# Performance work log

Hardware: AMD Instinct MI355X
Metric: run time of the kernel (lower is better)

The kernel has to match this reference:

```python
import jax, jax.numpy as jnp
import numpy as np

B, D, H1, H2, J, Q, O = 32768, 35, 256, 256, 12, 7, 5


def setup_inputs() -> dict:
    key = jax.random.key(0)
    ks = jax.random.split(key, 16)
    s = 0.05
    inp = {
        "x": jax.random.uniform(ks[0], (B, D), dtype=jnp.float32),
        "judge_ids": jax.random.randint(ks[1], (B,), 0, J, dtype=jnp.int32),
        # shared layers
        "W1_w": jax.random.normal(ks[2], (H1, D + 1), jnp.float32) * s,
        "W1_b": jnp.zeros((H1,), jnp.float32),
        "W2_w": jax.random.normal(ks[3], (H2, H1 + 1), jnp.float32) * s,
        "W2_b": jnp.zeros((H2,), jnp.float32),
        # judge-specific layers (stacked over J experts)
        "W1a_w": jax.random.normal(ks[4], (J, H1, D + 1), jnp.float32) * s,
        "W1a_b": jnp.zeros((J, H1), jnp.float32),
        "W2a_w": jax.random.normal(ks[5], (J, H2, H1 + 1), jnp.float32) * s,
        "W2a_b": jnp.zeros((J, H2), jnp.float32),
        # per-question output heads (shared + judge-specific)
        "V_w": jax.random.normal(ks[6], (Q, O, H2 + 1), jnp.float32) * s,
        "V_b": jnp.zeros((Q, O), jnp.float32),
        "Va_w": jax.random.normal(ks[7], (J, Q, O, H2 + 1), jnp.float32) * s,
        "Va_b": jnp.zeros((J, Q, O), jnp.float32),
    }
    return inp


def _append_ones(a):
    return jnp.concatenate([a, jnp.ones((a.shape[0], 1), a.dtype)], axis=1)


def reference(x, judge_ids, W1_w, W1_b, W2_w, W2_b, W1a_w, W1a_b, W2a_w, W2a_b, V_w, V_b, Va_w, Va_b):
    ids = judge_ids.astype(jnp.int32)
    xb = _append_ones(x)                                   # (B, D+1)
    # layer 1: shared + judge-routed
    a1 = jnp.einsum('bi,jhi->bjh', xb, W1a_w)              # (B, J, H1)
    j1 = jnp.take_along_axis(a1, ids[:, None, None], axis=1)[:, 0] + W1a_b[ids]
    z1 = jax.nn.relu(xb @ W1_w.T + W1_b + j1)              # (B, H1)
    z1b = _append_ones(z1)                                 # (B, H1+1)
    # layer 2
    a2 = jnp.einsum('bh,jgh->bjg', z1b, W2a_w)             # (B, J, H2)
    j2 = jnp.take_along_axis(a2, ids[:, None, None], axis=1)[:, 0] + W2a_b[ids]
    z2 = jax.nn.relu(z1b @ W2_w.T + W2_b + j2)             # (B, H2)
    z2b = _append_ones(z2)                                 # (B, H2+1)
    # per-question heads
    shared = jnp.einsum('bh,qoh->bqo', z2b, V_w) + V_b     # (B, Q, O)
    aV = jnp.einsum('bh,jqoh->bjqo', z2b, Va_w)            # (B, J, Q, O)
    jV = jnp.take_along_axis(aV, ids[:, None, None, None], axis=1)[:, 0] + Va_b[ids]
    return jax.nn.softmax(shared + jV, axis=-1)            # (B, Q, O)
```

## Files before the change

kernel.cpp:

```cpp
#include <hip/hip_runtime.h>
#include <stdint.h>

#define B_N   32768
#define D_IN  35
#define NJ    12
#define NQ    7
#define NO    5
#define QO    35
#define TILE  32
#define MAXSLOTS (B_N + NJ*TILE)
#define MAXT     (MAXSLOTS/TILE)

typedef __bf16  v8bf  __attribute__((ext_vector_type(8)));
typedef float   f32x4 __attribute__((ext_vector_type(4)));

__device__ __forceinline__ unsigned short f2bf(float f) {
    unsigned int u = __builtin_bit_cast(unsigned int, f);
    u += 0x7FFFu + ((u >> 16) & 1u);
    return (unsigned short)(u >> 16);
}
__device__ __forceinline__ unsigned int pack2(float a, float b) {
    return (unsigned int)f2bf(a) | ((unsigned int)f2bf(b) << 16);
}

__global__ void k_prep(const int* __restrict__ ids,
                       const float* __restrict__ W1_w, const float* __restrict__ W1_b,
                       const float* __restrict__ W2_w, const float* __restrict__ W2_b,
                       const float* __restrict__ W1a_w, const float* __restrict__ W1a_b,
                       const float* __restrict__ W2a_w, const float* __restrict__ W2a_b,
                       const float* __restrict__ V_w,  const float* __restrict__ V_b,
                       const float* __restrict__ Va_w, const float* __restrict__ Va_b,
                       unsigned short* __restrict__ w1c, unsigned short* __restrict__ w2c,
                       unsigned short* __restrict__ vc,
                       float* __restrict__ bias1, float* __restrict__ bias2,
                       float* __restrict__ biasv,
                       int* __restrict__ cursor, int* __restrict__ ntiles,
                       int* __restrict__ tileExpert, int* __restrict__ perm)
{
    const int tid = blockIdx.x * blockDim.x + threadIdx.x;
    const int nth = gridDim.x * blockDim.x;

    for (int q = tid; q < NJ * 256 * 64; q += nth) {
        int k4 = (q & 63) << 2, h = (q >> 6) & 255, jj = q >> 14;
        const float* a = &W2_w[h * 257 + k4];
        const float* b = &W2a_w[(jj * 256 + h) * 257 + k4];
        ushort4 o;
        o.x = f2bf(a[0] + b[0]); o.y = f2bf(a[1] + b[1]);
        o.z = f2bf(a[2] + b[2]); o.w = f2bf(a[3] + b[3]);
        *(ushort4*)&w2c[(size_t)q << 2] = o;
    }
    for (int q = tid; q < NJ * 256 * 16; q += nth) {
        int k4 = (q & 15) << 2, h = (q >> 4) & 255, jj = q >> 12;
        ushort4 o;
        float v[4];
#pragma unroll
        for (int e = 0; e < 4; ++e) {
            int k = k4 + e;
            v[e] = (k < D_IN) ? (W1_w[h * 36 + k] + W1a_w[(jj * 256 + h) * 36 + k]) : 0.f;
        }
        o.x = f2bf(v[0]); o.y = f2bf(v[1]); o.z = f2bf(v[2]); o.w = f2bf(v[3]);
        *(ushort4*)&w1c[(size_t)q << 2] = o;
    }
    for (int q = tid; q < NJ * 48 * 64; q += nth) {
        int k4 = (q & 63) << 2, qo = (q >> 6) % 48, jj = q / (48 * 64);
        ushort4 o;
        if (qo < QO) {
            const float* a = &V_w[qo * 257 + k4];
            const float* b = &Va_w[(jj * QO + qo) * 257 + k4];
            o.x = f2bf(a[0] + b[0]); o.y = f2bf(a[1] + b[1]);
            o.z = f2bf(a[2] + b[2]); o.w = f2bf(a[3] + b[3]);
        } else {
            o.x = o.y = o.z = o.w = 0;
        }
        *(ushort4*)&vc[(size_t)q << 2] = o;
    }
    for (int i = tid; i < NJ * 256; i += nth) {
        int h = i & 255, jj = i >> 8;
        bias1[i] = W1_w[h * 36 + 35] + W1a_w[(jj * 256 + h) * 36 + 35] + W1_b[h] + W1a_b[i];
        bias2[i] = W2_w[h * 257 + 256] + W2a_w[(jj * 256 + h) * 257 + 256] + W2_b[h] + W2a_b[i];
    }
    for (int i = tid; i < NJ * 48; i += nth) {
        int qo = i % 48, jj = i / 48;
        float v = 0.f;
        if (qo < QO) v = V_w[qo * 257 + 256] + Va_w[(jj * QO + qo) * 257 + 256]
                       + V_b[qo] + Va_b[jj * QO + qo];
        biasv[i] = v;
    }

    if (blockIdx.x == 0) {
        __shared__ int lh[NJ];
        __shared__ int s_cur[NJ], s_cnt[NJ], s_nt[NJ], tb[NJ + 1];
        const int lt = threadIdx.x;
        if (lt < NJ) lh[lt] = 0;
        __syncthreads();
        const int4* ids4 = (const int4*)ids;
        for (int i = lt; i < B_N / 4; i += 256) {
            int4 v = ids4[i];
            atomicAdd(&lh[v.x], 1); atomicAdd(&lh[v.y], 1);
            atomicAdd(&lh[v.z], 1); atomicAdd(&lh[v.w], 1);
        }
        __syncthreads();
        if (lt == 0) {
            int off = 0, t = 0;
            for (int j = 0; j < NJ; ++j) {
                int c = lh[j];
                int nt = (c + TILE - 1) / TILE;
                cursor[j] = off;
                s_cur[j] = off; s_cnt[j] = c; s_nt[j] = nt; tb[j] = t;
                t += nt;
                off += nt * TILE;
            }
            tb[NJ] = t;
            ntiles[0] = t;
        }
        __syncthreads();
        const int ntot = tb[NJ];
        for (int tt = lt; tt < ntot; tt += 256) {
            int j = 0;
            while (tb[j + 1] <= tt) ++j;
            tileExpert[tt] = j;
        }
        for (int p = lt; p < NJ * TILE; p += 256) {
            int j = p >> 5, o = p & 31;
            int c = s_cnt[j];
            int padN = s_nt[j] * TILE - c;
            if (o < padN) perm[s_cur[j] + c + o] = -1;
        }
    }
}

__global__ void k_scatter(const int* __restrict__ ids, int* __restrict__ cursor,
                          int* __restrict__ perm)
{
    __shared__ int lh[NJ], lbase[NJ];
    const int b = blockIdx.x * blockDim.x + threadIdx.x;
    if (threadIdx.x < NJ) lh[threadIdx.x] = 0;
    __syncthreads();
    int id = 0, rank = 0;
    if (b < B_N) { id = ids[b]; rank = atomicAdd(&lh[id], 1); }
    __syncthreads();
    if (threadIdx.x < NJ)
        lbase[threadIdx.x] = lh[threadIdx.x] ? atomicAdd(&cursor[threadIdx.x], lh[threadIdx.x]) : 0;
    __syncthreads();
    if (b < B_N) perm[lbase[id] + rank] = b;
}

__global__ __launch_bounds__(256, 4) void k_main(
    const float* __restrict__ x, float* __restrict__ out,
    const int* __restrict__ perm, const int* __restrict__ ntiles,
    const int* __restrict__ tileExpert,
    const unsigned short* __restrict__ w1c, const unsigned short* __restrict__ w2c,
    const unsigned short* __restrict__ vc,
    const float* __restrict__ bias1, const float* __restrict__ bias2,
    const float* __restrict__ biasv)
{
    __shared__ __align__(16) unsigned short s_z1[TILE][264];
    __shared__ __align__(16) union {
        unsigned short xb[TILE][72];
        float          lg[TILE][40];
    } s_u;
    __shared__ int s_rows[TILE];

    const int nt  = ntiles[0];
    const int bid = blockIdx.x;
    if (bid >= nt) return;

    const int q8 = nt >> 3, r8 = nt & 7;
    const int xcd = bid & 7, idx = bid >> 3;
    const int lbid = (xcd < r8 ? xcd * (q8 + 1) : r8 * (q8 + 1) + (xcd - r8) * q8) + idx;

    const int tid  = threadIdx.x;
    const int lane = tid & 63;
    const int wave = tid >> 6;
    const int l16  = lane & 15;
    const int lk   = lane >> 4;
    const int j    = tileExpert[lbid];

    const unsigned short* w1p = w1c + ((size_t)j << 14) + (size_t)(wave * 64) * 64;
    v8bf w1a0[4], w1a1[4];
#pragma unroll
    for (int t = 0; t < 4; ++t) {
        const unsigned short* rp = w1p + (t * 16 + l16) * 64;
        w1a0[t] = *(const v8bf*)&rp[lk * 8];
        w1a1[t] = *(const v8bf*)&rp[32 + lk * 8];
    }

    if (tid < TILE) s_rows[tid] = perm[lbid * TILE + tid];
    for (int i = tid; i < TILE * 36; i += 256) ((unsigned int*)s_u.xb)[i] = 0u;
    __syncthreads();

    for (int i = tid; i < TILE * D_IN; i += 256) {
        int s = i / D_IN, k = i - s * D_IN;
        int r = s_rows[s];
        s_u.xb[s][k] = f2bf(r >= 0 ? x[(size_t)r * D_IN + k] : 0.f);
    }
    __syncthreads();

    const f32x4 vz = {0.f, 0.f, 0.f, 0.f};

    {
        v8bf b1[2][2];
#pragma unroll
        for (int mt = 0; mt < 2; ++mt) {
            b1[mt][0] = *(const v8bf*)&s_u.xb[mt * 16 + l16][lk * 8];
            b1[mt][1] = *(const v8bf*)&s_u.xb[mt * 16 + l16][32 + lk * 8];
        }
        f32x4 acc[4][2];
#pragma unroll
        for (int t = 0; t < 4; ++t) { acc[t][0] = vz; acc[t][1] = vz; }
#pragma unroll
        for (int t = 0; t < 4; ++t) {
#pragma unroll
            for (int mt = 0; mt < 2; ++mt) {
                acc[t][mt] = __builtin_amdgcn_mfma_f32_16x16x32_bf16(w1a0[t], b1[mt][0], acc[t][mt], 0, 0, 0);
                acc[t][mt] = __builtin_amdgcn_mfma_f32_16x16x32_bf16(w1a1[t], b1[mt][1], acc[t][mt], 0, 0, 0);
            }
        }
        const unsigned short* w2p = w2c + ((size_t)j << 16) + (size_t)(wave * 64) * 256;
        v8bf a2pre[4];
#pragma unroll
        for (int gt = 0; gt < 4; ++gt)
            a2pre[gt] = *(const v8bf*)&w2p[(gt * 16 + l16) * 256 + lk * 8];

#pragma unroll
        for (int t = 0; t < 4; ++t) {
            f32x4 bz = *(const f32x4*)&bias1[j * 256 + wave * 64 + t * 16 + lk * 4];
#pragma unroll
            for (int mt = 0; mt < 2; ++mt) {
                float v0 = acc[t][mt][0] + bz[0], v1 = acc[t][mt][1] + bz[1];
                float v2 = acc[t][mt][2] + bz[2], v3 = acc[t][mt][3] + bz[3];
                v0 = v0 > 0.f ? v0 : 0.f; v1 = v1 > 0.f ? v1 : 0.f;
                v2 = v2 > 0.f ? v2 : 0.f; v3 = v3 > 0.f ? v3 : 0.f;
                uint2 pk; pk.x = pack2(v0, v1); pk.y = pack2(v2, v3);
                *(uint2*)&s_z1[mt * 16 + l16][wave * 64 + t * 16 + lk * 4] = pk;
            }
        }
        __syncthreads();

        f32x4 acc2[4][2];
#pragma unroll
        for (int gt = 0; gt < 4; ++gt) { acc2[gt][0] = vz; acc2[gt][1] = vz; }
        {
            v8bf bb0 = *(const v8bf*)&s_z1[l16][lk * 8];
            v8bf bb1 = *(const v8bf*)&s_z1[16 + l16][lk * 8];
#pragma unroll
            for (int gt = 0; gt < 4; ++gt) {
                acc2[gt][0] = __builtin_amdgcn_mfma_f32_16x16x32_bf16(a2pre[gt], bb0, acc2[gt][0], 0, 0, 0);
                acc2[gt][1] = __builtin_amdgcn_mfma_f32_16x16x32_bf16(a2pre[gt], bb1, acc2[gt][1], 0, 0, 0);
            }
        }
#pragma unroll 2
        for (int hc = 1; hc < 8; ++hc) {
            v8bf bb0 = *(const v8bf*)&s_z1[l16][hc * 32 + lk * 8];
            v8bf bb1 = *(const v8bf*)&s_z1[16 + l16][hc * 32 + lk * 8];
#pragma unroll
            for (int gt = 0; gt < 4; ++gt) {
                v8bf a = *(const v8bf*)&w2p[(gt * 16 + l16) * 256 + hc * 32 + lk * 8];
                acc2[gt][0] = __builtin_amdgcn_mfma_f32_16x16x32_bf16(a, bb0, acc2[gt][0], 0, 0, 0);
                acc2[gt][1] = __builtin_amdgcn_mfma_f32_16x16x32_bf16(a, bb1, acc2[gt][1], 0, 0, 0);
            }
        }
        const unsigned short* vp = vc + (size_t)j * 12288 + (size_t)(wave * 16) * 256;
        v8bf a3pre;
        if (wave < 3) a3pre = *(const v8bf*)&vp[l16 * 256 + lk * 8];

        __syncthreads();
#pragma unroll
        for (int gt = 0; gt < 4; ++gt) {
            f32x4 bz = *(const f32x4*)&bias2[j * 256 + wave * 64 + gt * 16 + lk * 4];
#pragma unroll
            for (int mt = 0; mt < 2; ++mt) {
                float v0 = acc2[gt][mt][0] + bz[0], v1 = acc2[gt][mt][1] + bz[1];
                float v2 = acc2[gt][mt][2] + bz[2], v3 = acc2[gt][mt][3] + bz[3];
                v0 = v0 > 0.f ? v0 : 0.f; v1 = v1 > 0.f ? v1 : 0.f;
                v2 = v2 > 0.f ? v2 : 0.f; v3 = v3 > 0.f ? v3 : 0.f;
                uint2 pk; pk.x = pack2(v0, v1); pk.y = pack2(v2, v3);
                *(uint2*)&s_z1[mt * 16 + l16][wave * 64 + gt * 16 + lk * 4] = pk;
            }
        }
        __syncthreads();

        if (wave < 3) {
            f32x4 av[2] = {vz, vz};
            {
                v8bf bb0 = *(const v8bf*)&s_z1[l16][lk * 8];
                v8bf bb1 = *(const v8bf*)&s_z1[16 + l16][lk * 8];
                av[0] = __builtin_amdgcn_mfma_f32_16x16x32_bf16(a3pre, bb0, av[0], 0, 0, 0);
                av[1] = __builtin_amdgcn_mfma_f32_16x16x32_bf16(a3pre, bb1, av[1], 0, 0, 0);
            }
#pragma unroll 4
            for (int gc = 1; gc < 8; ++gc) {
                v8bf bb0 = *(const v8bf*)&s_z1[l16][gc * 32 + lk * 8];
                v8bf bb1 = *(const v8bf*)&s_z1[16 + l16][gc * 32 + lk * 8];
                v8bf a = *(const v8bf*)&vp[l16 * 256 + gc * 32 + lk * 8];
                av[0] = __builtin_amdgcn_mfma_f32_16x16x32_bf16(a, bb0, av[0], 0, 0, 0);
                av[1] = __builtin_amdgcn_mfma_f32_16x16x32_bf16(a, bb1, av[1], 0, 0, 0);
            }
            int qb = wave * 16 + lk * 4;
            if (qb < 36) {
                f32x4 bz = *(const f32x4*)&biasv[j * 48 + qb];
#pragma unroll
                for (int mt = 0; mt < 2; ++mt) {
                    f32x4 v = av[mt] + bz;
                    *(f32x4*)&s_u.lg[mt * 16 + l16][qb] = v;
                }
            }
        }
    }
    __syncthreads();

    if (tid < TILE * NQ) {
        int s = tid / NQ, qq = tid - s * NQ;
        int r = s_rows[s];
        if (r >= 0) {
            float l[NO], mx = -1e30f;
#pragma unroll
            for (int o = 0; o < NO; ++o) {
                l[o] = s_u.lg[s][qq * NO + o];
                mx = l[o] > mx ? l[o] : mx;
            }
            float sum = 0.f, e[NO];
#pragma unroll
            for (int o = 0; o < NO; ++o) { e[o] = __expf(l[o] - mx); sum += e[o]; }
            float inv = 1.f / sum;
            float* op = out + (size_t)r * QO + qq * NO;
#pragma unroll
            for (int o = 0; o < NO; ++o) op[o] = e[o] * inv;
        }
    }
}

extern "C" void kernel_launch(void* const* d_in, const int* in_sizes, int n_in,
                              void* d_out, int out_size, void* d_ws, size_t ws_size,
                              hipStream_t stream)
{
    const float* x     = (const float*)d_in[0];
    const int*   ids   = (const int*)d_in[1];
    const float* W1_w  = (const float*)d_in[2];
    const float* W1_b  = (const float*)d_in[3];
    const float* W2_w  = (const float*)d_in[4];
    const float* W2_b  = (const float*)d_in[5];
    const float* W1a_w = (const float*)d_in[6];
    const float* W1a_b = (const float*)d_in[7];
    const float* W2a_w = (const float*)d_in[8];
    const float* W2a_b = (const float*)d_in[9];
    const float* V_w   = (const float*)d_in[10];
    const float* V_b   = (const float*)d_in[11];
    const float* Va_w  = (const float*)d_in[12];
    const float* Va_b  = (const float*)d_in[13];
    float* out = (float*)d_out;

    char* ws = (char*)d_ws;
    size_t off = 0;
    auto take = [&](size_t nbytes) -> void* {
        void* p = ws + off;
        off = (off + nbytes + 255) & ~(size_t)255;
        return p;
    };
    unsigned short* w1c = (unsigned short*)take((size_t)NJ * 256 * 64 * 2);
    unsigned short* w2c = (unsigned short*)take((size_t)NJ * 256 * 256 * 2);
    unsigned short* vc  = (unsigned short*)take((size_t)NJ * 48 * 256 * 2);
    float* bias1        = (float*)take((size_t)NJ * 256 * 4);
    float* bias2        = (float*)take((size_t)NJ * 256 * 4);
    float* biasv        = (float*)take((size_t)NJ * 48 * 4);
    int* cursor         = (int*)take(NJ * 4);
    int* ntiles         = (int*)take(4);
    int* tileExpert     = (int*)take(MAXT * 4);
    int* perm           = (int*)take((size_t)MAXSLOTS * 4);

    k_prep<<<768, 256, 0, stream>>>(ids, W1_w, W1_b, W2_w, W2_b, W1a_w, W1a_b,
                                    W2a_w, W2a_b, V_w, V_b, Va_w, Va_b,
                                    w1c, w2c, vc, bias1, bias2, biasv,
                                    cursor, ntiles, tileExpert, perm);
    k_scatter<<<(B_N + 255) / 256, 256, 0, stream>>>(ids, cursor, perm);
    k_main<<<MAXT, 256, 0, stream>>>(x, out, perm, ntiles, tileExpert,
                                     w1c, w2c, vc, bias1, bias2, biasv);
}
```

Baseline: 51.49 us.

## Double row tile to 64 with 512-thread blocks and register-based id histogram

Each block now processes 64 routed rows with 8 waves instead of 32 rows with 4. Each wave owns 32 output features instead of 64, and runs 4 row sub-tiles per MFMA weight fragment, so each loaded expert weight fragment is reused across twice as many rows. Separately, the expert-count histogram in the prep kernel now counts per-thread in registers and reduces with wave shuffles, replacing one LDS atomic per id. The trade-offs are about half as many blocks, more padding waste per expert, and higher register and LDS pressure per block.

```diff
diff --git a/kernel.cpp b/kernel.cpp
--- a/kernel.cpp
+++ b/kernel.cpp
@@ -7,7 +7,7 @@
 #define NQ    7
 #define NO    5
 #define QO    35
-#define TILE  32
+#define TILE  64
 #define MAXSLOTS (B_N + NJ*TILE)
 #define MAXT     (MAXSLOTS/TILE)
 
@@ -93,11 +93,22 @@
         const int lt = threadIdx.x;
         if (lt < NJ) lh[lt] = 0;
         __syncthreads();
+        int cnt[NJ];
+#pragma unroll
+        for (int j = 0; j < NJ; ++j) cnt[j] = 0;
         const int4* ids4 = (const int4*)ids;
         for (int i = lt; i < B_N / 4; i += 256) {
             int4 v = ids4[i];
-            atomicAdd(&lh[v.x], 1); atomicAdd(&lh[v.y], 1);
-            atomicAdd(&lh[v.z], 1); atomicAdd(&lh[v.w], 1);
+#pragma unroll
+            for (int j = 0; j < NJ; ++j)
+                cnt[j] += (v.x == j) + (v.y == j) + (v.z == j) + (v.w == j);
+        }
+#pragma unroll
+        for (int j = 0; j < NJ; ++j) {
+            int c = cnt[j];
+            c += __shfl_xor(c, 1);  c += __shfl_xor(c, 2);  c += __shfl_xor(c, 4);
+            c += __shfl_xor(c, 8);  c += __shfl_xor(c, 16); c += __shfl_xor(c, 32);
+            if ((lt & 63) == 0 && c) atomicAdd(&lh[j], c);
         }
         __syncthreads();
         if (lt == 0) {
@@ -121,7 +132,7 @@
             tileExpert[tt] = j;
         }
         for (int p = lt; p < NJ * TILE; p += 256) {
-            int j = p >> 5, o = p & 31;
+            int j = p / TILE, o = p % TILE;
             int c = s_cnt[j];
             int padN = s_nt[j] * TILE - c;
             if (o < padN) perm[s_cur[j] + c + o] = -1;
@@ -145,7 +156,7 @@
     if (b < B_N) perm[lbase[id] + rank] = b;
 }
 
-__global__ __launch_bounds__(256, 4) void k_main(
+__global__ __launch_bounds__(512, 4) void k_main(
     const float* __restrict__ x, float* __restrict__ out,
     const int* __restrict__ perm, const int* __restrict__ ntiles,
     const int* __restrict__ tileExpert,
@@ -176,20 +187,20 @@
     const int lk   = lane >> 4;
     const int j    = tileExpert[lbid];
 
-    const unsigned short* w1p = w1c + ((size_t)j << 14) + (size_t)(wave * 64) * 64;
-    v8bf w1a0[4], w1a1[4];
-#pragma unroll
-    for (int t = 0; t < 4; ++t) {
+    const unsigned short* w1p = w1c + ((size_t)j << 14) + (size_t)(wave * 32) * 64;
+    v8bf w1a0[2], w1a1[2];
+#pragma unroll
+    for (int t = 0; t < 2; ++t) {
         const unsigned short* rp = w1p + (t * 16 + l16) * 64;
         w1a0[t] = *(const v8bf*)&rp[lk * 8];
         w1a1[t] = *(const v8bf*)&rp[32 + lk * 8];
     }
 
     if (tid < TILE) s_rows[tid] = perm[lbid * TILE + tid];
-    for (int i = tid; i < TILE * 36; i += 256) ((unsigned int*)s_u.xb)[i] = 0u;
-    __syncthreads();
-
-    for (int i = tid; i < TILE * D_IN; i += 256) {
+    for (int i = tid; i < TILE * 36; i += 512) ((unsigned int*)s_u.xb)[i] = 0u;
+    __syncthreads();
+
+    for (int i = tid; i < TILE * D_IN; i += 512) {
         int s = i / D_IN, k = i - s * D_IN;
         int r = s_rows[s];
         s_u.xb[s][k] = f2bf(r >= 0 ? x[(size_t)r * D_IN + k] : 0.f);
@@ -199,65 +210,74 @@
     const f32x4 vz = {0.f, 0.f, 0.f, 0.f};
 
     {
-        v8bf b1[2][2];
-#pragma unroll
-        for (int mt = 0; mt < 2; ++mt) {
+        v8bf b1[4][2];
+#pragma unroll
+        for (int mt = 0; mt < 4; ++mt) {
             b1[mt][0] = *(const v8bf*)&s_u.xb[mt * 16 + l16][lk * 8];
             b1[mt][1] = *(const v8bf*)&s_u.xb[mt * 16 + l16][32 + lk * 8];
         }
-        f32x4 acc[4][2];
-#pragma unroll
-        for (int t = 0; t < 4; ++t) { acc[t][0] = vz; acc[t][1] = vz; }
-#pragma unroll
-        for (int t = 0; t < 4; ++t) {
-#pragma unroll
-            for (int mt = 0; mt < 2; ++mt) {
+        f32x4 acc[2][4];
+#pragma unroll
+        for (int t = 0; t < 2; ++t)
+#pragma unroll
+            for (int mt = 0; mt < 4; ++mt) acc[t][mt] = vz;
+#pragma unroll
+        for (int t = 0; t < 2; ++t) {
+#pragma unroll
+            for (int mt = 0; mt < 4; ++mt) {
                 acc[t][mt] = __builtin_amdgcn_mfma_f32_16x16x32_bf16(w1a0[t], b1[mt][0], acc[t][mt], 0, 0, 0);
                 acc[t][mt] = __builtin_amdgcn_mfma_f32_16x16x32_bf16(w1a1[t], b1[mt][1], acc[t][mt], 0, 0, 0);
             }
         }
-        const unsigned short* w2p = w2c + ((size_t)j << 16) + (size_t)(wave * 64) * 256;
-        v8bf a2pre[4];
-#pragma unroll
-        for (int gt = 0; gt < 4; ++gt)
+        const unsigned short* w2p = w2c + ((size_t)j << 16) + (size_t)(wave * 32) * 256;
+        v8bf a2pre[2];
+#pragma unroll
+        for (int gt = 0; gt < 2; ++gt)
             a2pre[gt] = *(const v8bf*)&w2p[(gt * 16 + l16) * 256 + lk * 8];
 
 #pragma unroll
-        for (int t = 0; t < 4; ++t) {
-            f32x4 bz = *(const f32x4*)&bias1[j * 256 + wave * 64 + t * 16 + lk * 4];
-#pragma unroll
-            for (int mt = 0; mt < 2; ++mt) {
+        for (int t = 0; t < 2; ++t) {
+            f32x4 bz = *(const f32x4*)&bias1[j * 256 + wave * 32 + t * 16 + lk * 4];
+#pragma unroll
+            for (int mt = 0; mt < 4; ++mt) {
                 float v0 = acc[t][mt][0] + bz[0], v1 = acc[t][mt][1] + bz[1];
                 float v2 = acc[t][mt][2] + bz[2], v3 = acc[t][mt][3] + bz[3];
                 v0 = v0 > 0.f ? v0 : 0.f; v1 = v1 > 0.f ? v1 : 0.f;
                 v2 = v2 > 0.f ? v2 : 0.f; v3 = v3 > 0.f ? v3 : 0.f;
                 uint2 pk; pk.x = pack2(v0, v1); pk.y = pack2(v2, v3);
-                *(uint2*)&s_z1[mt * 16 + l16][wave * 64 + t * 16 + lk * 4] = pk;
-            }
-        }
-        __syncthreads();
-
-        f32x4 acc2[4][2];
-#pragma unroll
-        for (int gt = 0; gt < 4; ++gt) { acc2[gt][0] = vz; acc2[gt][1] = vz; }
+                *(uint2*)&s_z1[mt * 16 + l16][wave * 32 + t * 16 + lk * 4] = pk;
+            }
+        }
+        __syncthreads();
+
+        f32x4 acc2[2][4];
+#pragma unroll
+        for (int gt = 0; gt < 2; ++gt)
+#pragma unroll
+            for (int mt = 0; mt < 4; ++mt) acc2[gt][mt] = vz;
         {
-            v8bf bb0 = *(const v8bf*)&s_z1[l16][lk * 8];
-            v8bf bb1 = *(const v8bf*)&s_z1[16 + l16][lk * 8];
-#pragma unroll
-            for (int gt = 0; gt < 4; ++gt) {
-                acc2[gt][0] = __builtin_amdgcn_mfma_f32_16x16x32_bf16(a2pre[gt], bb0, acc2[gt][0], 0, 0, 0);
-                acc2[gt][1] = __builtin_amdgcn_mfma_f32_16x16x32_bf16(a2pre[gt], bb1, acc2[gt][1], 0, 0, 0);
-            }
-        }
-#pragma unroll 2
+            v8bf bb[4];
+#pragma unroll
+            for (int mt = 0; mt < 4; ++mt)
+                bb[mt] = *(const v8bf*)&s_z1[mt * 16 + l16][lk * 8];
+#pragma unroll
+            for (int gt = 0; gt < 2; ++gt)
+#pragma unroll
+                for (int mt = 0; mt < 4; ++mt)
+                    acc2[gt][mt] = __builtin_amdgcn_mfma_f32_16x16x32_bf16(a2pre[gt], bb[mt], acc2[gt][mt], 0, 0, 0);
+        }
+#pragma unroll 1
         for (int hc = 1; hc < 8; ++hc) {
-            v8bf bb0 = *(const v8bf*)&s_z1[l16][hc * 32 + lk * 8];
-            v8bf bb1 = *(const v8bf*)&s_z1[16 + l16][hc * 32 + lk * 8];
-#pragma unroll
-            for (int gt = 0; gt < 4; ++gt) {
+            v8bf bb[4];
+#pragma unroll
+            for (int mt = 0; mt < 4; ++mt)
+                bb[mt] = *(const v8bf*)&s_z1[mt * 16 + l16][hc * 32 + lk * 8];
+#pragma unroll
+            for (int gt = 0; gt < 2; ++gt) {
                 v8bf a = *(const v8bf*)&w2p[(gt * 16 + l16) * 256 + hc * 32 + lk * 8];
-                acc2[gt][0] = __builtin_amdgcn_mfma_f32_16x16x32_bf16(a, bb0, acc2[gt][0], 0, 0, 0);
-                acc2[gt][1] = __builtin_amdgcn_mfma_f32_16x16x32_bf16(a, bb1, acc2[gt][1], 0, 0, 0);
+#pragma unroll
+                for (int mt = 0; mt < 4; ++mt)
+                    acc2[gt][mt] = __builtin_amdgcn_mfma_f32_16x16x32_bf16(a, bb[mt], acc2[gt][mt], 0, 0, 0);
             }
         }
         const unsigned short* vp = vc + (size_t)j * 12288 + (size_t)(wave * 16) * 256;
@@ -266,41 +286,43 @@
 
         __syncthreads();
 #pragma unroll
-        for (int gt = 0; gt < 4; ++gt) {
-            f32x4 bz = *(const f32x4*)&bias2[j * 256 + wave * 64 + gt * 16 + lk * 4];
-#pragma unroll
-            for (int mt = 0; mt < 2; ++mt) {
+        for (int gt = 0; gt < 2; ++gt) {
+            f32x4 bz = *(const f32x4*)&bias2[j * 256 + wave * 32 + gt * 16 + lk * 4];
+#pragma unroll
+            for (int mt = 0; mt < 4; ++mt) {
                 float v0 = acc2[gt][mt][0] + bz[0], v1 = acc2[gt][mt][1] + bz[1];
                 float v2 = acc2[gt][mt][2] + bz[2], v3 = acc2[gt][mt][3] + bz[3];
                 v0 = v0 > 0.f ? v0 : 0.f; v1 = v1 > 0.f ? v1 : 0.f;
                 v2 = v2 > 0.f ? v2 : 0.f; v3 = v3 > 0.f ? v3 : 0.f;
                 uint2 pk; pk.x = pack2(v0, v1); pk.y = pack2(v2, v3);
-                *(uint2*)&s_z1[mt * 16 + l16][wave * 64 + gt * 16 + lk * 4] = pk;
+                *(uint2*)&s_z1[mt * 16 + l16][wave * 32 + gt * 16 + lk * 4] = pk;
             }
         }
         __syncthreads();
 
         if (wave < 3) {
-            f32x4 av[2] = {vz, vz};
+            f32x4 av[4] = {vz, vz, vz, vz};
             {
-                v8bf bb0 = *(const v8bf*)&s_z1[l16][lk * 8];
-                v8bf bb1 = *(const v8bf*)&s_z1[16 + l16][lk * 8];
-                av[0] = __builtin_amdgcn_mfma_f32_16x16x32_bf16(a3pre, bb0, av[0], 0, 0, 0);
-                av[1] = __builtin_amdgcn_mfma_f32_16x16x32_bf16(a3pre, bb1, av[1], 0, 0, 0);
-            }
-#pragma unroll 4
+#pragma unroll
+                for (int mt = 0; mt < 4; ++mt) {
+                    v8bf bb = *(const v8bf*)&s_z1[mt * 16 + l16][lk * 8];
+                    av[mt] = __builtin_amdgcn_mfma_f32_16x16x32_bf16(a3pre, bb, av[mt], 0, 0, 0);
+                }
+            }
+#pragma unroll 1
             for (int gc = 1; gc < 8; ++gc) {
-                v8bf bb0 = *(const v8bf*)&s_z1[l16][gc * 32 + lk * 8];
-                v8bf bb1 = *(const v8bf*)&s_z1[16 + l16][gc * 32 + lk * 8];
                 v8bf a = *(const v8bf*)&vp[l16 * 256 + gc * 32 + lk * 8];
-                av[0] = __builtin_amdgcn_mfma_f32_16x16x32_bf16(a, bb0, av[0], 0, 0, 0);
-                av[1] = __builtin_amdgcn_mfma_f32_16x16x32_bf16(a, bb1, av[1], 0, 0, 0);
+#pragma unroll
+                for (int mt = 0; mt < 4; ++mt) {
+                    v8bf bb = *(const v8bf*)&s_z1[mt * 16 + l16][gc * 32 + lk * 8];
+                    av[mt] = __builtin_amdgcn_mfma_f32_16x16x32_bf16(a, bb, av[mt], 0, 0, 0);
+                }
             }
             int qb = wave * 16 + lk * 4;
             if (qb < 36) {
                 f32x4 bz = *(const f32x4*)&biasv[j * 48 + qb];
 #pragma unroll
-                for (int mt = 0; mt < 2; ++mt) {
+                for (int mt = 0; mt < 4; ++mt) {
                     f32x4 v = av[mt] + bz;
                     *(f32x4*)&s_u.lg[mt * 16 + l16][qb] = v;
                 }
@@ -373,6 +395,6 @@
                                     w1c, w2c, vc, bias1, bias2, biasv,
                                     cursor, ntiles, tileExpert, perm);
     k_scatter<<<(B_N + 255) / 256, 256, 0, stream>>>(ids, cursor, perm);
-    k_main<<<MAXT, 256, 0, stream>>>(x, out, perm, ntiles, tileExpert,
+    k_main<<<MAXT, 512, 0, stream>>>(x, out, perm, ntiles, tileExpert,
                                      w1c, w2c, vc, bias1, bias2, biasv);
 }
```

Result: slower. 55.72 us (+8.2%).
